# Kernel optimization log

Measured on AMD Instinct MI355X. Metric: run time of the kernel, lower is better.

## Reference

```python
import jax, jax.numpy as jnp
import numpy as np

N = 100_000        # number of independent Markov chains (particles)
N_FRAMES = 500     # chain length (module default)
# index 0 -> identity (stay), index 1 -> swap (flip state)
T_MAT = jnp.array([[[1., 0.], [0., 1.]],
                   [[0., 1.], [1., 0.]]], dtype=jnp.float32)


def setup_inputs() -> dict:
    key = jax.random.key(0)
    idx = jax.random.randint(key, (N,), 0, 2)
    initial = jax.nn.one_hot(idx, 2, dtype=jnp.float32)  # one-hot states [N,2]
    return {"initial": initial, "seed": 0}


def reference(initial, seed):
    key = jax.random.key(seed)
    kp, ks = jax.random.split(key)
    # torch code resets transition probs once at i==0 with p = rand()*0.001
    p = jax.random.uniform(kp, (), dtype=jnp.float32) * 0.001
    # row 0: [0.8, 0.2]; row 1: [1-p, p]
    p1 = jnp.stack([jnp.float32(0.2), p])  # P(class==1) per categorical row
    keys = jax.random.split(ks, N_FRAMES)

    def step(state, k):
        # Categorical sample per (particle, row): A[n, j] ~ Bernoulli(p1[j])
        u = jax.random.uniform(k, state.shape, dtype=state.dtype)
        A = (u < p1[None, :]).astype(state.dtype)          # [N,2] in {0,1}
        t = jnp.sum(state * A, axis=-1).astype(jnp.int32)  # [N] select action
        m = T_MAT[t]                                       # [N,2,2] permutation
        new_state = jnp.einsum('nc,ncd->nd', state, m)     # [N,2]
        return new_state, new_state

    _, chain = jax.lax.scan(step, initial, keys)
    return chain  # [N_FRAMES, N, 2]
```

## Files before the change

kernel.cpp:

```cpp
#include <hip/hip_runtime.h>
#include <stdint.h>

#define N_PART   100000
#define N_FRAMES 500

__device__ __forceinline__ uint32_t rotl32(uint32_t v, int d) {
    return (v << d) | (v >> (32 - d));
}

#define TF_ROUND(r) { x0 += x1; x1 = rotl32(x1, (r)); x1 ^= x0; }

__device__ __forceinline__ void tf2x32(uint32_t k0, uint32_t k1,
                                       uint32_t x0, uint32_t x1,
                                       uint32_t &o0, uint32_t &o1) {
    const uint32_t k2 = k0 ^ k1 ^ 0x1BD11BDAu;
    x0 += k0; x1 += k1;
    TF_ROUND(13) TF_ROUND(15) TF_ROUND(26) TF_ROUND(6)
    x0 += k1; x1 += k2 + 1u;
    TF_ROUND(17) TF_ROUND(29) TF_ROUND(16) TF_ROUND(24)
    x0 += k2; x1 += k0 + 2u;
    TF_ROUND(13) TF_ROUND(15) TF_ROUND(26) TF_ROUND(6)
    x0 += k0; x1 += k1 + 3u;
    TF_ROUND(17) TF_ROUND(29) TF_ROUND(16) TF_ROUND(24)
    x0 += k1; x1 += k2 + 4u;
    TF_ROUND(13) TF_ROUND(15) TF_ROUND(26) TF_ROUND(6)
    x0 += k2; x1 += k0 + 5u;
    o0 = x0; o1 = x1;
}

__device__ __forceinline__ float uniform_from_bits(uint32_t bits) {
    return __uint_as_float((bits >> 9) | 0x3f800000u) - 1.0f;
}

__global__ __launch_bounds__(256)
void hmm_kernel(const float* __restrict__ initial,
                const int* __restrict__ seed_ptr,
                float* __restrict__ out) {
    __shared__ uint32_t skey0[N_FRAMES];
    __shared__ uint32_t skey1[N_FRAMES];
    __shared__ float sp;

    const int tid = threadIdx.x;
    const uint32_t seed_lo = (uint32_t)seed_ptr[0];
    const uint32_t seed_hi = 0u;

    uint32_t ks0, ks1;
    tf2x32(seed_hi, seed_lo, 0u, 1u, ks0, ks1);

    for (int t = tid; t < N_FRAMES; t += blockDim.x) {
        uint32_t a, b;
        tf2x32(ks0, ks1, 0u, (uint32_t)t, a, b);
        skey0[t] = a;
        skey1[t] = b;
    }
    if (tid == 0) {
        uint32_t kp0, kp1, b0, b1;
        tf2x32(seed_hi, seed_lo, 0u, 0u, kp0, kp1);
        tf2x32(kp0, kp1, 0u, 0u, b0, b1);
        sp = uniform_from_bits(b0 ^ b1) * 0.001f;
    }
    __syncthreads();

    const int n = blockIdx.x * blockDim.x + tid;
    if (n >= N_PART) return;

    const float p  = sp;
    const float p0 = 0.2f;

    int s = (initial[2 * n + 1] > 0.5f) ? 1 : 0;
    const uint32_t base = 2u * (uint32_t)n;

    float2* __restrict__ outv = (float2*)out;
    const float2 oh0 = make_float2(1.0f, 0.0f);
    const float2 oh1 = make_float2(0.0f, 1.0f);

    for (int t = 0; t < N_FRAMES; t += 2) {
        const uint32_t ka0 = skey0[t],     ka1 = skey1[t];
        const uint32_t kb0 = skey0[t + 1], kb1 = skey1[t + 1];

        uint32_t a0, a1, c00, c01, c10, c11;
        tf2x32(ka0, ka1, 0u, base + (uint32_t)s, a0, a1);
        tf2x32(kb0, kb1, 0u, base,               c00, c01);
        tf2x32(kb0, kb1, 0u, base + 1u,          c10, c11);

        const float uA = uniform_from_bits(a0 ^ a1);
        s ^= (uA < (s ? p : p0)) ? 1 : 0;
        outv[(size_t)t * N_PART + n] = s ? oh1 : oh0;

        const float uB = uniform_from_bits(s ? (c10 ^ c11) : (c00 ^ c01));
        s ^= (uB < (s ? p : p0)) ? 1 : 0;
        outv[(size_t)(t + 1) * N_PART + n] = s ? oh1 : oh0;
    }
}

extern "C" void kernel_launch(void* const* d_in, const int* in_sizes, int n_in,
                              void* d_out, int out_size, void* d_ws, size_t ws_size,
                              hipStream_t stream) {
    const float* initial = (const float*)d_in[0];
    const int*   seed    = (const int*)d_in[1];
    float*       out     = (float*)d_out;

    const int block = 256;
    const int grid = (N_PART + block - 1) / block;
    hmm_kernel<<<grid, block, 0, stream>>>(initial, seed, out);
}
```

Before: 534.0 us.

## Parallelize chain over time via per-chunk transition maps and prefix composition

Splits the 500-step sequential chain into 32 chunks of 16 frames. A first kernel computes per-particle, per-frame transition maps, packs them into 2-bit fields and composes a chunk-level state map. A second kernel resolves each chunk's starting state by applying the preceding chunk maps and then writes the one-hot outputs. This exposes far more parallelism than the single serial per-particle loop, at the cost of generating both random draws per frame (previously only one for half the steps) plus workspace traffic and a second launch.

Result: slower. 630.5 us (+18.1%).

```diff
diff --git a/kernel.cpp b/kernel.cpp
--- a/kernel.cpp
+++ b/kernel.cpp
@@ -3,6 +3,8 @@
 
 #define N_PART   100000
 #define N_FRAMES 500
+#define FPW      16
+#define NW       32
 
 __device__ __forceinline__ uint32_t rotl32(uint32_t v, int d) {
     return (v << d) | (v >> (32 - d));
@@ -32,64 +34,94 @@
     return __uint_as_float((bits >> 9) | 0x3f800000u) - 1.0f;
 }
 
+__device__ __forceinline__ uint32_t compose_map(uint32_t m2, uint32_t m1) {
+    const uint32_t a = (m2 >> (m1 & 1u)) & 1u;
+    const uint32_t b = (m2 >> ((m1 >> 1) & 1u)) & 1u;
+    return a | (b << 1);
+}
+
 __global__ __launch_bounds__(256)
-void hmm_kernel(const float* __restrict__ initial,
-                const int* __restrict__ seed_ptr,
-                float* __restrict__ out) {
-    __shared__ uint32_t skey0[N_FRAMES];
-    __shared__ uint32_t skey1[N_FRAMES];
-    __shared__ float sp;
+void map_kernel(const int* __restrict__ seed_ptr,
+                uint32_t* __restrict__ words,
+                uint8_t* __restrict__ cmap) {
+    __shared__ uint32_t sk0[FPW], sk1[FPW];
+    __shared__ float sp_;
 
+    const int w   = blockIdx.y;
     const int tid = threadIdx.x;
     const uint32_t seed_lo = (uint32_t)seed_ptr[0];
-    const uint32_t seed_hi = 0u;
 
-    uint32_t ks0, ks1;
-    tf2x32(seed_hi, seed_lo, 0u, 1u, ks0, ks1);
-
-    for (int t = tid; t < N_FRAMES; t += blockDim.x) {
-        uint32_t a, b;
-        tf2x32(ks0, ks1, 0u, (uint32_t)t, a, b);
-        skey0[t] = a;
-        skey1[t] = b;
+    if (tid < FPW) {
+        uint32_t ks0, ks1, a, b;
+        tf2x32(0u, seed_lo, 0u, 1u, ks0, ks1);
+        tf2x32(ks0, ks1, 0u, (uint32_t)(w * FPW + tid), a, b);
+        sk0[tid] = a; sk1[tid] = b;
     }
-    if (tid == 0) {
+    if (tid == 32) {
         uint32_t kp0, kp1, b0, b1;
-        tf2x32(seed_hi, seed_lo, 0u, 0u, kp0, kp1);
+        tf2x32(0u, seed_lo, 0u, 0u, kp0, kp1);
         tf2x32(kp0, kp1, 0u, 0u, b0, b1);
-        sp = uniform_from_bits(b0 ^ b1) * 0.001f;
+        sp_ = uniform_from_bits(b0 ^ b1) * 0.001f;
     }
     __syncthreads();
 
     const int n = blockIdx.x * blockDim.x + tid;
     if (n >= N_PART) return;
 
-    const float p  = sp;
-    const float p0 = 0.2f;
+    const float p = sp_;
+    const uint32_t base = 2u * (uint32_t)n;
+    const int nf = min(FPW, N_FRAMES - w * FPW);
 
-    int s = (initial[2 * n + 1] > 0.5f) ? 1 : 0;
-    const uint32_t base = 2u * (uint32_t)n;
+    uint32_t word = 0u;
+    uint32_t cm = 2u;
+    for (int f = 0; f < FPW; ++f) {
+        uint32_t m;
+        if (f < nf) {
+            uint32_t a0, a1, b0, b1;
+            tf2x32(sk0[f], sk1[f], 0u, base,      a0, a1);
+            tf2x32(sk0[f], sk1[f], 0u, base + 1u, b0, b1);
+            const float u0 = uniform_from_bits(a0 ^ a1);
+            const float u1 = uniform_from_bits(b0 ^ b1);
+            const uint32_t A0 = (u0 < 0.2f) ? 1u : 0u;
+            const uint32_t B1 = (u1 < p)    ? 0u : 1u;
+            m = A0 | (B1 << 1);
+        } else {
+            m = 2u;
+        }
+        word |= m << (2 * f);
+        cm = compose_map(m, cm);
+    }
+    words[(size_t)w * N_PART + n] = word;
+    cmap [(size_t)w * N_PART + n] = (uint8_t)cm;
+}
 
+__global__ __launch_bounds__(256)
+void emit_kernel(const float* __restrict__ initial,
+                 const uint32_t* __restrict__ words,
+                 const uint8_t* __restrict__ cmap,
+                 float* __restrict__ out) {
+    const int w   = blockIdx.y;
+    const int tid = threadIdx.x;
+    const int n   = blockIdx.x * blockDim.x + tid;
+    if (n >= N_PART) return;
+
+    uint32_t s = (initial[2 * n + 1] > 0.5f) ? 1u : 0u;
+    for (int j = 0; j < w; ++j)
+        s = ((uint32_t)cmap[(size_t)j * N_PART + n] >> s) & 1u;
+
+    const uint32_t word = words[(size_t)w * N_PART + n];
     float2* __restrict__ outv = (float2*)out;
     const float2 oh0 = make_float2(1.0f, 0.0f);
     const float2 oh1 = make_float2(0.0f, 1.0f);
+    const int t0 = w * FPW;
+    const int nf = min(FPW, N_FRAMES - t0);
 
-    for (int t = 0; t < N_FRAMES; t += 2) {
-        const uint32_t ka0 = skey0[t],     ka1 = skey1[t];
-        const uint32_t kb0 = skey0[t + 1], kb1 = skey1[t + 1];
-
-        uint32_t a0, a1, c00, c01, c10, c11;
-        tf2x32(ka0, ka1, 0u, base + (uint32_t)s, a0, a1);
-        tf2x32(kb0, kb1, 0u, base,               c00, c01);
-        tf2x32(kb0, kb1, 0u, base + 1u,          c10, c11);
-
-        const float uA = uniform_from_bits(a0 ^ a1);
-        s ^= (uA < (s ? p : p0)) ? 1 : 0;
-        outv[(size_t)t * N_PART + n] = s ? oh1 : oh0;
-
-        const float uB = uniform_from_bits(s ? (c10 ^ c11) : (c00 ^ c01));
-        s ^= (uB < (s ? p : p0)) ? 1 : 0;
-        outv[(size_t)(t + 1) * N_PART + n] = s ? oh1 : oh0;
+    #pragma unroll
+    for (int f = 0; f < FPW; ++f) {
+        if (f < nf) {
+            s = (word >> (2 * f + s)) & 1u;
+            outv[(size_t)(t0 + f) * N_PART + n] = s ? oh1 : oh0;
+        }
     }
 }
 
@@ -100,7 +132,11 @@
     const int*   seed    = (const int*)d_in[1];
     float*       out     = (float*)d_out;
 
+    uint32_t* words = (uint32_t*)d_ws;
+    uint8_t*  cmap  = (uint8_t*)(words + (size_t)NW * N_PART);
+
     const int block = 256;
-    const int grid = (N_PART + block - 1) / block;
-    hmm_kernel<<<grid, block, 0, stream>>>(initial, seed, out);
+    dim3 grid((N_PART + block - 1) / block, NW);
+    map_kernel <<<grid, block, 0, stream>>>(seed, words, cmap);
+    emit_kernel<<<grid, block, 0, stream>>>(initial, words, cmap, out);
 }
```
